# Performance work log

Measured on AMD Instinct MI355X. Metric: run time of the kernel, lower is better.

Reference implementation:

```python
import jax, jax.numpy as jnp
import numpy as np

HIDDEN = 1024
NUM_HEADS = 16
HEAD_DIM = HIDDEN // NUM_HEADS


def setup_inputs() -> dict:
    key = jax.random.key(0)
    ks = jax.random.split(key, 10)
    B, T, S = 2, 2048, 2048
    sc = 1.0 / np.sqrt(HIDDEN)
    inp = {
        "tgt": jax.random.normal(ks[0], (B, T, HIDDEN), jnp.float32),
        "src": jax.random.normal(ks[1], (B, S, HIDDEN), jnp.float32),
        # per-head projection weights stacked: [H, in_dim, head_dim]
        "Wq": jax.random.normal(ks[2], (NUM_HEADS, HIDDEN, HEAD_DIM), jnp.float32) * sc,
        "bq": jnp.zeros((NUM_HEADS, HEAD_DIM), jnp.float32),
        "Wk": jax.random.normal(ks[3], (NUM_HEADS, HIDDEN, HEAD_DIM), jnp.float32) * sc,
        "bk": jnp.zeros((NUM_HEADS, HEAD_DIM), jnp.float32),
        "Wv": jax.random.normal(ks[4], (NUM_HEADS, HIDDEN, HEAD_DIM), jnp.float32) * sc,
        "bv": jnp.zeros((NUM_HEADS, HEAD_DIM), jnp.float32),
        "Wo": jax.random.normal(ks[5], (HIDDEN, HIDDEN), jnp.float32) * sc,
        "bo": jnp.zeros((HIDDEN,), jnp.float32),
    }
    return inp


def reference(tgt, src, Wq, bq, Wk, bk, Wv, bv, Wo, bo):
    # Per-head linear projections (vectorized over heads)
    q = jnp.einsum("btd,hdk->bhtk", tgt, Wq) + bq[None, :, None, :]  # [B,H,T,Dh]
    k = jnp.einsum("bsd,hdk->bhsk", src, Wk) + bk[None, :, None, :]  # [B,H,S,Dh]
    v = jnp.einsum("bsd,hdk->bhsk", src, Wv) + bv[None, :, None, :]  # [B,H,S,Dh]
    scale = 1.0 / jnp.sqrt(jnp.asarray(HEAD_DIM, q.dtype))
    scores = jnp.einsum("bhtk,bhsk->bhts", q, k) * scale  # [B,H,T,S]
    weights = jax.nn.softmax(scores, axis=-1)
    out = jnp.einsum("bhts,bhsk->bhtk", weights, v)  # [B,H,T,Dh]
    # concat heads along last dim (head order matches torch cat)
    B, H, T, Dh = out.shape
    h = out.transpose(0, 2, 1, 3).reshape(B, T, H * Dh)
    return h @ Wo + bo
```

## Files before the change

kernel.cpp:

```cpp
#include <hip/hip_runtime.h>

typedef _Float16 f16;
typedef __attribute__((ext_vector_type(4))) _Float16 f16x4;
typedef __attribute__((ext_vector_type(8))) _Float16 f16x8;
typedef __attribute__((ext_vector_type(4))) float f32x4;

constexpr int HID = 1024, NH = 16, DH = 64, BB = 2, TT = 2048, SS = 2048;
constexpr float SCL = 0.18033688011112042f;

__device__ __forceinline__ void gl_lds16(const void* g, void* l) {
  __builtin_amdgcn_global_load_lds(
      (const __attribute__((address_space(1))) void*)g,
      (__attribute__((address_space(3))) void*)l, 16, 0, 0);
}

#define VMCNT(N) asm volatile("s_waitcnt vmcnt(" #N ")" ::: "memory")

#if __has_builtin(__builtin_amdgcn_exp2f)
#define EXP2(x) __builtin_amdgcn_exp2f(x)
#else
#define EXP2(x) exp2f(x)
#endif

__global__ __launch_bounds__(256) void k_cvt_act_all(
    const float* __restrict__ tgt, const float* __restrict__ src,
    f16* __restrict__ tgt16, f16* __restrict__ src16) {
  const int n_each = BB * TT * HID;
  int i = (blockIdx.x * 256 + threadIdx.x) * 8;
  const float* in = tgt;
  f16* out = tgt16;
  if (i >= n_each) { in = src; out = src16; i -= n_each; }
  float4 a = *(const float4*)(in + i);
  float4 b = *(const float4*)(in + i + 4);
  f16x8 o;
  o[0] = (f16)a.x; o[1] = (f16)a.y; o[2] = (f16)a.z; o[3] = (f16)a.w;
  o[4] = (f16)b.x; o[5] = (f16)b.y; o[6] = (f16)b.z; o[7] = (f16)b.w;
  *(f16x8*)(out + i) = o;
}

__global__ __launch_bounds__(256) void k_cvt_w_all(
    const float* __restrict__ Wq, const float* __restrict__ Wk,
    const float* __restrict__ Wv, const float* __restrict__ Wo,
    f16* __restrict__ wq16, f16* __restrict__ wk16, f16* __restrict__ wv16,
    f16* __restrict__ wo16) {
  __shared__ f16 t[64 * 72];
  const int x = blockIdx.x, wsel = x >> 8, idx = x & 255;
  const float* in;
  f16* out;
  int C, c0, d0, slab;
  float scale = 1.0f;
  if (wsel < 3) {
    in = (wsel == 0) ? Wq : ((wsel == 1) ? Wk : Wv);
    out = (wsel == 0) ? wq16 : ((wsel == 1) ? wk16 : wv16);
    if (wsel == 0) scale = SCL;
    C = 64; c0 = 0; d0 = (idx & 15) * 64; slab = idx >> 4;
  } else {
    in = Wo; out = wo16;
    C = 1024; c0 = (idx & 15) * 64; d0 = (idx >> 4) * 64; slab = 0;
  }
  const float* ip = in + (size_t)slab * 1024 * C;
  int tid = threadIdx.x;
  int r = tid >> 4, cq = (tid & 15) * 4;
  for (int rr = 0; rr < 64; rr += 16) {
    float4 v = *(const float4*)(ip + (size_t)(d0 + r + rr) * C + (c0 + cq));
    t[(cq + 0) * 72 + r + rr] = (f16)(v.x * scale);
    t[(cq + 1) * 72 + r + rr] = (f16)(v.y * scale);
    t[(cq + 2) * 72 + r + rr] = (f16)(v.z * scale);
    t[(cq + 3) * 72 + r + rr] = (f16)(v.w * scale);
  }
  __syncthreads();
  int c = tid >> 2, dq = (tid & 3) * 16;
  f16* op = out + (size_t)(slab * C + c0 + c) * 1024 + d0 + dq;
  *(f16x8*)op = *(const f16x8*)&t[c * 72 + dq];
  *(f16x8*)(op + 8) = *(const f16x8*)&t[c * 72 + dq + 8];
}

__global__ __launch_bounds__(256) void k_gemm_qkv(
    const f16* __restrict__ tgt16, const f16* __restrict__ src16,
    const f16* __restrict__ wq, const f16* __restrict__ wk,
    const f16* __restrict__ wv, const float* __restrict__ bq,
    const float* __restrict__ bk, const float* __restrict__ bv,
    f16* __restrict__ Qo, f16* __restrict__ Ko, f16* __restrict__ Vo) {
  __shared__ f16 lA[2][128 * 64];
  __shared__ f16 lB[2][128 * 64];
  const int tid = threadIdx.x;
  const int lane = tid & 63, hi = lane >> 4, t16 = lane & 15;
  const int w = tid >> 6;
  const int wr = (w >> 1) * 64, wc = (w & 1) * 64;
  const int i = blockIdx.x;
  const int xcd = i & 7, j = i >> 3;
  const int z = j >> 5, r = j & 31;
  const int m0 = (xcd * 4 + (r & 3)) * 128, n0 = (r >> 2) * 128;
  const f16* A = z ? src16 : tgt16;
  const f16* Bt = (z == 0) ? wq : ((z == 1) ? wk : wv);
  const float* bias = (z == 0) ? bq : ((z == 1) ? bk : bv);
  const float bscale = (z == 0) ? SCL : 1.0f;

  f32x4 acc[4][4];
#pragma unroll
  for (int a = 0; a < 4; a++)
#pragma unroll
    for (int bb = 0; bb < 4; bb++) acc[a][bb] = (f32x4){0.f, 0.f, 0.f, 0.f};

  auto STAGE = [&](int s, int kt) {
#pragma unroll
    for (int it = 0; it < 4; ++it) {
      int u = it * 256 + tid, row = u >> 3, un = u & 7;
      int gc = kt * 64 + ((un ^ (row & 7)) << 3);
      gl_lds16(A + (size_t)(m0 + row) * 1024 + gc, (char*)&lA[s][0] + u * 16);
      gl_lds16(Bt + (size_t)(n0 + row) * 1024 + gc, (char*)&lB[s][0] + u * 16);
    }
  };

  STAGE(0, 0);
  VMCNT(0);
  __builtin_amdgcn_s_barrier();
  int cur = 0;
  for (int kt = 0; kt < 16; ++kt) {
    if (kt < 15) STAGE(cur ^ 1, kt + 1);
#pragma unroll
    for (int ks = 0; ks < 2; ++ks) {
      f16x8 af[4], bf[4];
#pragma unroll
      for (int mi = 0; mi < 4; mi++) {
        int rr = wr + mi * 16 + t16;
        af[mi] = *(const f16x8*)&lA[cur][rr * 64 + (((ks * 4 + hi) ^ (rr & 7)) << 3)];
      }
#pragma unroll
      for (int ni = 0; ni < 4; ni++) {
        int rr = wc + ni * 16 + t16;
        bf[ni] = *(const f16x8*)&lB[cur][rr * 64 + (((ks * 4 + hi) ^ (rr & 7)) << 3)];
      }
      __builtin_amdgcn_s_setprio(1);
#pragma unroll
      for (int mi = 0; mi < 4; mi++)
#pragma unroll
        for (int ni = 0; ni < 4; ni++)
          acc[mi][ni] = __builtin_amdgcn_mfma_f32_16x16x32_f16(
              af[mi], bf[ni], acc[mi][ni], 0, 0, 0);
      __builtin_amdgcn_s_setprio(0);
    }
    VMCNT(0);
    __builtin_amdgcn_s_barrier();
    cur ^= 1;
  }

  if (z < 2) {
    f16* outp = z ? Ko : Qo;
#pragma unroll
    for (int mi = 0; mi < 4; mi++)
#pragma unroll
      for (int ni = 0; ni < 4; ni++)
#pragma unroll
        for (int rg = 0; rg < 4; rg++) {
          int m = m0 + wr + mi * 16 + hi * 4 + rg;
          int n = n0 + wc + ni * 16 + t16;
          outp[(size_t)m * 1024 + n] = (f16)(acc[mi][ni][rg] + bias[n] * bscale);
        }
  } else {
#pragma unroll
    for (int mi = 0; mi < 4; mi++)
#pragma unroll
      for (int ni = 0; ni < 4; ni++)
#pragma unroll
        for (int rg = 0; rg < 4; rg++) {
          int m = m0 + wr + mi * 16 + hi * 4 + rg;
          int n = n0 + wc + ni * 16 + t16;
          int b = m >> 11, s = m & 2047;
          Vo[(((size_t)(b * NH + (n >> 6)) * DH + (n & 63)) << 11) + s] =
              (f16)(acc[mi][ni][rg] + bias[n]);
        }
  }
}

__global__ __launch_bounds__(256) void k_gemm_o(const f16* __restrict__ A,
                                                const f16* __restrict__ Bt,
                                                const float* __restrict__ bias,
                                                float* __restrict__ outp) {
  __shared__ f16 lA[2][128 * 64];
  __shared__ f16 lB[2][64 * 64];
  const int tid = threadIdx.x;
  const int lane = tid & 63, hi = lane >> 4, t16 = lane & 15;
  const int w = tid >> 6;
  const int wr = (w >> 1) * 64, wc = (w & 1) * 32;
  const int i = blockIdx.x;
  const int xcd = i & 7, j = i >> 3;
  const int m0 = (xcd * 4 + (j & 3)) * 128, n0 = (j >> 2) * 64;

  f32x4 acc[4][2];
#pragma unroll
  for (int a = 0; a < 4; a++)
#pragma unroll
    for (int bb = 0; bb < 2; bb++) acc[a][bb] = (f32x4){0.f, 0.f, 0.f, 0.f};

  auto STAGE = [&](int s, int kt) {
#pragma unroll
    for (int it = 0; it < 4; ++it) {
      int u = it * 256 + tid, row = u >> 3, un = u & 7;
      int gc = kt * 64 + ((un ^ (row & 7)) << 3);
      gl_lds16(A + (size_t)(m0 + row) * 1024 + gc, (char*)&lA[s][0] + u * 16);
    }
#pragma unroll
    for (int it = 0; it < 2; ++it) {
      int u = it * 256 + tid, row = u >> 3, un = u & 7;
      int gc = kt * 64 + ((un ^ (row & 7)) << 3);
      gl_lds16(Bt + (size_t)(n0 + row) * 1024 + gc, (char*)&lB[s][0] + u * 16);
    }
  };

  STAGE(0, 0);
  VMCNT(0);
  __builtin_amdgcn_s_barrier();
  int cur = 0;
  for (int kt = 0; kt < 16; ++kt) {
    if (kt < 15) STAGE(cur ^ 1, kt + 1);
#pragma unroll
    for (int ks = 0; ks < 2; ++ks) {
      f16x8 af[4], bf[2];
#pragma unroll
      for (int mi = 0; mi < 4; mi++) {
        int rr = wr + mi * 16 + t16;
        af[mi] = *(const f16x8*)&lA[cur][rr * 64 + (((ks * 4 + hi) ^ (rr & 7)) << 3)];
      }
#pragma unroll
      for (int ni = 0; ni < 2; ni++) {
        int rr = wc + ni * 16 + t16;
        bf[ni] = *(const f16x8*)&lB[cur][rr * 64 + (((ks * 4 + hi) ^ (rr & 7)) << 3)];
      }
      __builtin_amdgcn_s_setprio(1);
#pragma unroll
      for (int mi = 0; mi < 4; mi++)
#pragma unroll
        for (int ni = 0; ni < 2; ni++)
          acc[mi][ni] = __builtin_amdgcn_mfma_f32_16x16x32_f16(
              af[mi], bf[ni], acc[mi][ni], 0, 0, 0);
      __builtin_amdgcn_s_setprio(0);
    }
    VMCNT(0);
    __builtin_amdgcn_s_barrier();
    cur ^= 1;
  }

#pragma unroll
  for (int mi = 0; mi < 4; mi++)
#pragma unroll
    for (int ni = 0; ni < 2; ni++)
#pragma unroll
      for (int rg = 0; rg < 4; rg++) {
        int m = m0 + wr + mi * 16 + hi * 4 + rg;
        int n = n0 + wc + ni * 16 + t16;
        outp[(size_t)m * 1024 + n] = acc[mi][ni][rg] + bias[n];
      }
}

__global__ __launch_bounds__(256) void k_attn(const f16* __restrict__ Q,
                                              const f16* __restrict__ K,
                                              const f16* __restrict__ Vt,
                                              f16* __restrict__ Hout) {
  __shared__ f16 lK[3][64 * 64];
  __shared__ f16 lV[3][64 * 64];
  const int tid = threadIdx.x;
  const int lane = tid & 63, hi = lane >> 4, t16 = lane & 15;
  const int w = tid >> 6;
  const int id = blockIdx.y * 16 + blockIdx.x;
  const int bh = (id & 7) * 4 + ((id >> 3) & 3);
  const int b = bh >> 4, h = bh & 15;
  const int tq = (id >> 5) * 128 + w * 32;

  f16x8 qa[2][2];
#pragma unroll
  for (int g = 0; g < 2; ++g)
#pragma unroll
    for (int ks = 0; ks < 2; ++ks)
      qa[g][ks] = *(const f16x8*)(Q + (size_t)(b * TT + tq + g * 16 + t16) * HID +
                                  h * DH + ks * 32 + hi * 8);
#pragma unroll
  for (int g = 0; g < 2; ++g)
#pragma unroll
    for (int ks = 0; ks < 2; ++ks) asm volatile("" : "+v"(qa[g][ks]));

  float lrow[2] = {0.f, 0.f};
  f32x4 o[2][4];
#pragma unroll
  for (int g = 0; g < 2; ++g)
#pragma unroll
    for (int dc = 0; dc < 4; ++dc) o[g][dc] = (f32x4){0.f, 0.f, 0.f, 0.f};

  auto STAGE = [&](int s, int sb) {
#pragma unroll
    for (int it = 0; it < 2; ++it) {
      int u = it * 256 + tid, row = u >> 3, un = u & 7;
      int kc = (un ^ (row & 7)) << 3;
      gl_lds16(K + (size_t)(b * SS + sb * 64 + row) * HID + h * DH + kc,
               (char*)&lK[s][0] + u * 16);
      gl_lds16(Vt + ((size_t)(b * NH + h) * DH + row) * SS + sb * 64 + kc,
               (char*)&lV[s][0] + u * 16);
    }
  };

  STAGE(0, 0);
  STAGE(1, 1);
  int cs = 0;
  for (int i = 0; i < 32; ++i) {
    if (i < 31) { VMCNT(4); } else { VMCNT(0); }
    __builtin_amdgcn_s_barrier();
    __builtin_amdgcn_sched_barrier(0);
    int ns = cs + 2; if (ns >= 3) ns -= 3;
    if (i + 2 < 32) STAGE(ns, i + 2);

    f16x8 kb[4][2];
#pragma unroll
    for (int sb = 0; sb < 4; ++sb) {
      int r = sb * 16 + t16;
#pragma unroll
      for (int ks = 0; ks < 2; ++ks)
        kb[sb][ks] = *(const f16x8*)&lK[cs][r * 64 + (((ks * 4 + hi) ^ (r & 7)) << 3)];
    }
    f32x4 sc[4][2];
#pragma unroll
    for (int sb = 0; sb < 4; ++sb)
#pragma unroll
      for (int g = 0; g < 2; ++g) sc[sb][g] = (f32x4){0.f, 0.f, 0.f, 0.f};
    __builtin_amdgcn_s_setprio(1);
#pragma unroll
    for (int sb = 0; sb < 4; ++sb)
#pragma unroll
      for (int g = 0; g < 2; ++g)
#pragma unroll
        for (int ks = 0; ks < 2; ++ks)
          sc[sb][g] = __builtin_amdgcn_mfma_f32_16x16x32_f16(
              kb[sb][ks], qa[g][ks], sc[sb][g], 0, 0, 0);
    __builtin_amdgcn_s_setprio(0);

    f16x4 pf[2][4];
#pragma unroll
    for (int g = 0; g < 2; ++g) {
#pragma unroll
      for (int sb = 0; sb < 4; ++sb) {
        float p0 = EXP2(sc[sb][g][0]);
        float p1 = EXP2(sc[sb][g][1]);
        float p2 = EXP2(sc[sb][g][2]);
        float p3 = EXP2(sc[sb][g][3]);
        lrow[g] += (p0 + p1) + (p2 + p3);
        f16x4 pv; pv[0] = (f16)p0; pv[1] = (f16)p1; pv[2] = (f16)p2; pv[3] = (f16)p3;
        pf[g][sb] = pv;
      }
    }

    f16x4 vf[4][4];
#pragma unroll
    for (int dc = 0; dc < 4; ++dc) {
#pragma unroll
      for (int sk = 0; sk < 4; ++sk) {
        int chunk = ((2 * sk + (hi >> 1)) ^ (t16 & 7));
        vf[dc][sk] = *(const f16x4*)&lV[cs][(dc * 16 + t16) * 64 + chunk * 8 + (hi & 1) * 4];
      }
    }

    __builtin_amdgcn_s_setprio(1);
#pragma unroll
    for (int g = 0; g < 2; ++g)
#pragma unroll
      for (int dc = 0; dc < 4; ++dc)
#pragma unroll
        for (int sk = 0; sk < 4; ++sk)
          o[g][dc] = __builtin_amdgcn_mfma_f32_16x16x16f16(vf[dc][sk], pf[g][sk],
                                                           o[g][dc], 0, 0, 0);
    __builtin_amdgcn_s_setprio(0);

    cs = (cs == 2) ? 0 : cs + 1;
  }

#pragma unroll
  for (int g = 0; g < 2; ++g) {
    float l = lrow[g];
    l += __shfl_xor(l, 16);
    l += __shfl_xor(l, 32);
    float rinv = 1.0f / l;
#pragma unroll
    for (int dc = 0; dc < 4; ++dc) {
      f16x4 ov;
#pragma unroll
      for (int rg = 0; rg < 4; ++rg) ov[rg] = (f16)(o[g][dc][rg] * rinv);
      *(f16x4*)(Hout + (size_t)(b * TT + tq + g * 16 + t16) * HID + h * DH +
                dc * 16 + hi * 4) = ov;
    }
  }
}

extern "C" void kernel_launch(void* const* d_in, const int* in_sizes, int n_in,
                              void* d_out, int out_size, void* d_ws, size_t ws_size,
                              hipStream_t stream) {
  const float* tgt = (const float*)d_in[0];
  const float* src = (const float*)d_in[1];
  const float* Wq = (const float*)d_in[2];
  const float* bq = (const float*)d_in[3];
  const float* Wk = (const float*)d_in[4];
  const float* bk = (const float*)d_in[5];
  const float* Wv = (const float*)d_in[6];
  const float* bv = (const float*)d_in[7];
  const float* Wo = (const float*)d_in[8];
  const float* bo = (const float*)d_in[9];
  float* out = (float*)d_out;

  char* ws = (char*)d_ws;
  f16* tgt16 = (f16*)(ws);
  f16* src16 = (f16*)(ws + (8u << 20));
  f16* wq16 = (f16*)(ws + (16u << 20));
  f16* wk16 = (f16*)(ws + (18u << 20));
  f16* wv16 = (f16*)(ws + (20u << 20));
  f16* wo16 = (f16*)(ws + (22u << 20));
  f16* Q16 = (f16*)(ws + (24u << 20));
  f16* K16 = (f16*)(ws + (32u << 20));
  f16* Vt16 = (f16*)(ws + (40u << 20));
  f16* h16 = (f16*)(ws + (48u << 20));

  k_cvt_act_all<<<4096, 256, 0, stream>>>(tgt, src, tgt16, src16);
  k_cvt_w_all<<<1024, 256, 0, stream>>>(Wq, Wk, Wv, Wo, wq16, wk16, wv16, wo16);

  k_gemm_qkv<<<768, 256, 0, stream>>>(tgt16, src16, wq16, wk16, wv16,
                                      bq, bk, bv, Q16, K16, Vt16);

  k_attn<<<dim3(16, 32), 256, 0, stream>>>(Q16, K16, Vt16, h16);

  k_gemm_o<<<512, 256, 0, stream>>>(h16, wo16, bo, out);
}
```

Measured before the change: 212.7 us.

## Merge convert kernels, shrink QKV GEMM N-tile, use 128-key double-buffered attention tiles

Three separate changes. The activation and weight fp16 conversion kernels become one launch, removing a kernel boundary. The QKV GEMM tile goes from 128x128 to 128x64, doubling the grid to 1536 blocks for better CU occupancy and load balance at the cost of more A-tile reloads. The attention kernel switches from a 3-stage 64-key pipeline to a 2-stage 128-key double buffer with one barrier per 128 keys. That fills LDS with larger tiles, possibly lowering occupancy, and the loads get less prefetch lead time.

```diff
diff --git a/kernel.cpp b/kernel.cpp
--- a/kernel.cpp
+++ b/kernel.cpp
@@ -22,29 +22,29 @@
 #define EXP2(x) exp2f(x)
 #endif
 
-__global__ __launch_bounds__(256) void k_cvt_act_all(
+__global__ __launch_bounds__(256) void k_cvt_all(
     const float* __restrict__ tgt, const float* __restrict__ src,
-    f16* __restrict__ tgt16, f16* __restrict__ src16) {
-  const int n_each = BB * TT * HID;
-  int i = (blockIdx.x * 256 + threadIdx.x) * 8;
-  const float* in = tgt;
-  f16* out = tgt16;
-  if (i >= n_each) { in = src; out = src16; i -= n_each; }
-  float4 a = *(const float4*)(in + i);
-  float4 b = *(const float4*)(in + i + 4);
-  f16x8 o;
-  o[0] = (f16)a.x; o[1] = (f16)a.y; o[2] = (f16)a.z; o[3] = (f16)a.w;
-  o[4] = (f16)b.x; o[5] = (f16)b.y; o[6] = (f16)b.z; o[7] = (f16)b.w;
-  *(f16x8*)(out + i) = o;
-}
-
-__global__ __launch_bounds__(256) void k_cvt_w_all(
     const float* __restrict__ Wq, const float* __restrict__ Wk,
     const float* __restrict__ Wv, const float* __restrict__ Wo,
-    f16* __restrict__ wq16, f16* __restrict__ wk16, f16* __restrict__ wv16,
-    f16* __restrict__ wo16) {
+    f16* __restrict__ tgt16, f16* __restrict__ src16, f16* __restrict__ wq16,
+    f16* __restrict__ wk16, f16* __restrict__ wv16, f16* __restrict__ wo16) {
   __shared__ f16 t[64 * 72];
-  const int x = blockIdx.x, wsel = x >> 8, idx = x & 255;
+  const int bx = blockIdx.x;
+  if (bx < 4096) {
+    const int n_each = BB * TT * HID;
+    int i = (bx * 256 + threadIdx.x) * 8;
+    const float* in = tgt;
+    f16* out = tgt16;
+    if (i >= n_each) { in = src; out = src16; i -= n_each; }
+    float4 a = *(const float4*)(in + i);
+    float4 b = *(const float4*)(in + i + 4);
+    f16x8 o;
+    o[0] = (f16)a.x; o[1] = (f16)a.y; o[2] = (f16)a.z; o[3] = (f16)a.w;
+    o[4] = (f16)b.x; o[5] = (f16)b.y; o[6] = (f16)b.z; o[7] = (f16)b.w;
+    *(f16x8*)(out + i) = o;
+    return;
+  }
+  const int x = bx - 4096, wsel = x >> 8, idx = x & 255;
   const float* in;
   f16* out;
   int C, c0, d0, slab;
@@ -82,25 +82,25 @@
     const float* __restrict__ bk, const float* __restrict__ bv,
     f16* __restrict__ Qo, f16* __restrict__ Ko, f16* __restrict__ Vo) {
   __shared__ f16 lA[2][128 * 64];
-  __shared__ f16 lB[2][128 * 64];
+  __shared__ f16 lB[2][64 * 64];
   const int tid = threadIdx.x;
   const int lane = tid & 63, hi = lane >> 4, t16 = lane & 15;
   const int w = tid >> 6;
-  const int wr = (w >> 1) * 64, wc = (w & 1) * 64;
+  const int wr = (w >> 1) * 64, wc = (w & 1) * 32;
   const int i = blockIdx.x;
   const int xcd = i & 7, j = i >> 3;
-  const int z = j >> 5, r = j & 31;
-  const int m0 = (xcd * 4 + (r & 3)) * 128, n0 = (r >> 2) * 128;
+  const int z = j >> 6, r = j & 63;
+  const int m0 = (xcd * 4 + (r & 3)) * 128, n0 = (r >> 2) * 64;
   const f16* A = z ? src16 : tgt16;
   const f16* Bt = (z == 0) ? wq : ((z == 1) ? wk : wv);
   const float* bias = (z == 0) ? bq : ((z == 1) ? bk : bv);
   const float bscale = (z == 0) ? SCL : 1.0f;
 
-  f32x4 acc[4][4];
+  f32x4 acc[4][2];
 #pragma unroll
   for (int a = 0; a < 4; a++)
 #pragma unroll
-    for (int bb = 0; bb < 4; bb++) acc[a][bb] = (f32x4){0.f, 0.f, 0.f, 0.f};
+    for (int bb = 0; bb < 2; bb++) acc[a][bb] = (f32x4){0.f, 0.f, 0.f, 0.f};
 
   auto STAGE = [&](int s, int kt) {
 #pragma unroll
@@ -108,6 +108,11 @@
       int u = it * 256 + tid, row = u >> 3, un = u & 7;
       int gc = kt * 64 + ((un ^ (row & 7)) << 3);
       gl_lds16(A + (size_t)(m0 + row) * 1024 + gc, (char*)&lA[s][0] + u * 16);
+    }
+#pragma unroll
+    for (int it = 0; it < 2; ++it) {
+      int u = it * 256 + tid, row = u >> 3, un = u & 7;
+      int gc = kt * 64 + ((un ^ (row & 7)) << 3);
       gl_lds16(Bt + (size_t)(n0 + row) * 1024 + gc, (char*)&lB[s][0] + u * 16);
     }
   };
@@ -120,14 +125,14 @@
     if (kt < 15) STAGE(cur ^ 1, kt + 1);
 #pragma unroll
     for (int ks = 0; ks < 2; ++ks) {
-      f16x8 af[4], bf[4];
+      f16x8 af[4], bf[2];
 #pragma unroll
       for (int mi = 0; mi < 4; mi++) {
         int rr = wr + mi * 16 + t16;
         af[mi] = *(const f16x8*)&lA[cur][rr * 64 + (((ks * 4 + hi) ^ (rr & 7)) << 3)];
       }
 #pragma unroll
-      for (int ni = 0; ni < 4; ni++) {
+      for (int ni = 0; ni < 2; ni++) {
         int rr = wc + ni * 16 + t16;
         bf[ni] = *(const f16x8*)&lB[cur][rr * 64 + (((ks * 4 + hi) ^ (rr & 7)) << 3)];
       }
@@ -135,7 +140,7 @@
 #pragma unroll
       for (int mi = 0; mi < 4; mi++)
 #pragma unroll
-        for (int ni = 0; ni < 4; ni++)
+        for (int ni = 0; ni < 2; ni++)
           acc[mi][ni] = __builtin_amdgcn_mfma_f32_16x16x32_f16(
               af[mi], bf[ni], acc[mi][ni], 0, 0, 0);
       __builtin_amdgcn_s_setprio(0);
@@ -150,7 +155,7 @@
 #pragma unroll
     for (int mi = 0; mi < 4; mi++)
 #pragma unroll
-      for (int ni = 0; ni < 4; ni++)
+      for (int ni = 0; ni < 2; ni++)
 #pragma unroll
         for (int rg = 0; rg < 4; rg++) {
           int m = m0 + wr + mi * 16 + hi * 4 + rg;
@@ -161,7 +166,7 @@
 #pragma unroll
     for (int mi = 0; mi < 4; mi++)
 #pragma unroll
-      for (int ni = 0; ni < 4; ni++)
+      for (int ni = 0; ni < 2; ni++)
 #pragma unroll
         for (int rg = 0; rg < 4; rg++) {
           int m = m0 + wr + mi * 16 + hi * 4 + rg;
@@ -257,8 +262,8 @@
                                               const f16* __restrict__ K,
                                               const f16* __restrict__ Vt,
                                               f16* __restrict__ Hout) {
-  __shared__ f16 lK[3][64 * 64];
-  __shared__ f16 lV[3][64 * 64];
+  __shared__ f16 lK[2][128 * 64];
+  __shared__ f16 lV[2][64 * 128];
   const int tid = threadIdx.x;
   const int lane = tid & 63, hi = lane >> 4, t16 = lane & 15;
   const int w = tid >> 6;
@@ -286,89 +291,95 @@
 #pragma unroll
     for (int dc = 0; dc < 4; ++dc) o[g][dc] = (f32x4){0.f, 0.f, 0.f, 0.f};
 
-  auto STAGE = [&](int s, int sb) {
-#pragma unroll
-    for (int it = 0; it < 2; ++it) {
+  auto STAGE = [&](int s, int tb) {
+#pragma unroll
+    for (int it = 0; it < 4; ++it) {
       int u = it * 256 + tid, row = u >> 3, un = u & 7;
       int kc = (un ^ (row & 7)) << 3;
-      gl_lds16(K + (size_t)(b * SS + sb * 64 + row) * HID + h * DH + kc,
+      gl_lds16(K + (size_t)(b * SS + tb * 128 + row) * HID + h * DH + kc,
                (char*)&lK[s][0] + u * 16);
-      gl_lds16(Vt + ((size_t)(b * NH + h) * DH + row) * SS + sb * 64 + kc,
+    }
+#pragma unroll
+    for (int it = 0; it < 4; ++it) {
+      int u = it * 256 + tid, d = u >> 4, un = u & 15;
+      int scol = ((un & 8) | ((un & 7) ^ (d & 7))) << 3;
+      gl_lds16(Vt + ((size_t)(b * NH + h) * DH + d) * SS + tb * 128 + scol,
                (char*)&lV[s][0] + u * 16);
     }
   };
 
   STAGE(0, 0);
-  STAGE(1, 1);
-  int cs = 0;
-  for (int i = 0; i < 32; ++i) {
-    if (i < 31) { VMCNT(4); } else { VMCNT(0); }
+  VMCNT(0);
+  __builtin_amdgcn_s_barrier();
+  int cur = 0;
+  for (int t = 0; t < 16; ++t) {
+    if (t < 15) STAGE(cur ^ 1, t + 1);
+#pragma unroll
+    for (int hs = 0; hs < 2; ++hs) {
+      f16x8 kb[4][2];
+#pragma unroll
+      for (int sb = 0; sb < 4; ++sb) {
+        int r = hs * 64 + sb * 16 + t16;
+#pragma unroll
+        for (int ks = 0; ks < 2; ++ks)
+          kb[sb][ks] = *(const f16x8*)&lK[cur][r * 64 + (((ks * 4 + hi) ^ (r & 7)) << 3)];
+      }
+      f32x4 sc[4][2];
+#pragma unroll
+      for (int sb = 0; sb < 4; ++sb)
+#pragma unroll
+        for (int g = 0; g < 2; ++g) sc[sb][g] = (f32x4){0.f, 0.f, 0.f, 0.f};
+      __builtin_amdgcn_s_setprio(1);
+#pragma unroll
+      for (int sb = 0; sb < 4; ++sb)
+#pragma unroll
+        for (int g = 0; g < 2; ++g)
+#pragma unroll
+          for (int ks = 0; ks < 2; ++ks)
+            sc[sb][g] = __builtin_amdgcn_mfma_f32_16x16x32_f16(
+                kb[sb][ks], qa[g][ks], sc[sb][g], 0, 0, 0);
+      __builtin_amdgcn_s_setprio(0);
+
+      f16x4 pf[2][4];
+#pragma unroll
+      for (int g = 0; g < 2; ++g) {
+#pragma unroll
+        for (int sb = 0; sb < 4; ++sb) {
+          float p0 = EXP2(sc[sb][g][0]);
+          float p1 = EXP2(sc[sb][g][1]);
+          float p2 = EXP2(sc[sb][g][2]);
+          float p3 = EXP2(sc[sb][g][3]);
+          lrow[g] += (p0 + p1) + (p2 + p3);
+          f16x4 pv; pv[0] = (f16)p0; pv[1] = (f16)p1; pv[2] = (f16)p2; pv[3] = (f16)p3;
+          pf[g][sb] = pv;
+        }
+      }
+
+      f16x4 vf[4][4];
+#pragma unroll
+      for (int dc = 0; dc < 4; ++dc) {
+#pragma unroll
+        for (int sk = 0; sk < 4; ++sk) {
+          int chunk = ((2 * sk + (hi >> 1)) ^ (t16 & 7));
+          vf[dc][sk] = *(const f16x4*)&lV[cur][(dc * 16 + t16) * 128 + hs * 64 +
+                                               chunk * 8 + (hi & 1) * 4];
+        }
+      }
+
+      __builtin_amdgcn_s_setprio(1);
+#pragma unroll
+      for (int g = 0; g < 2; ++g)
+#pragma unroll
+        for (int dc = 0; dc < 4; ++dc)
+#pragma unroll
+          for (int sk = 0; sk < 4; ++sk)
+            o[g][dc] = __builtin_amdgcn_mfma_f32_16x16x16f16(vf[dc][sk], pf[g][sk],
+                                                             o[g][dc], 0, 0, 0);
+      __builtin_amdgcn_s_setprio(0);
+    }
+    VMCNT(0);
     __builtin_amdgcn_s_barrier();
-    __builtin_amdgcn_sched_barrier(0);
-    int ns = cs + 2; if (ns >= 3) ns -= 3;
-    if (i + 2 < 32) STAGE(ns, i + 2);
-
-    f16x8 kb[4][2];
-#pragma unroll
-    for (int sb = 0; sb < 4; ++sb) {
-      int r = sb * 16 + t16;
-#pragma unroll
-      for (int ks = 0; ks < 2; ++ks)
-        kb[sb][ks] = *(const f16x8*)&lK[cs][r * 64 + (((ks * 4 + hi) ^ (r & 7)) << 3)];
-    }
-    f32x4 sc[4][2];
-#pragma unroll
-    for (int sb = 0; sb < 4; ++sb)
-#pragma unroll
-      for (int g = 0; g < 2; ++g) sc[sb][g] = (f32x4){0.f, 0.f, 0.f, 0.f};
-    __builtin_amdgcn_s_setprio(1);
-#pragma unroll
-    for (int sb = 0; sb < 4; ++sb)
-#pragma unroll
-      for (int g = 0; g < 2; ++g)
-#pragma unroll
-        for (int ks = 0; ks < 2; ++ks)
-          sc[sb][g] = __builtin_amdgcn_mfma_f32_16x16x32_f16(
-              kb[sb][ks], qa[g][ks], sc[sb][g], 0, 0, 0);
-    __builtin_amdgcn_s_setprio(0);
-
-    f16x4 pf[2][4];
-#pragma unroll
-    for (int g = 0; g < 2; ++g) {
-#pragma unroll
-      for (int sb = 0; sb < 4; ++sb) {
-        float p0 = EXP2(sc[sb][g][0]);
-        float p1 = EXP2(sc[sb][g][1]);
-        float p2 = EXP2(sc[sb][g][2]);
-        float p3 = EXP2(sc[sb][g][3]);
-        lrow[g] += (p0 + p1) + (p2 + p3);
-        f16x4 pv; pv[0] = (f16)p0; pv[1] = (f16)p1; pv[2] = (f16)p2; pv[3] = (f16)p3;
-        pf[g][sb] = pv;
-      }
-    }
-
-    f16x4 vf[4][4];
-#pragma unroll
-    for (int dc = 0; dc < 4; ++dc) {
-#pragma unroll
-      for (int sk = 0; sk < 4; ++sk) {
-        int chunk = ((2 * sk + (hi >> 1)) ^ (t16 & 7));
-        vf[dc][sk] = *(const f16x4*)&lV[cs][(dc * 16 + t16) * 64 + chunk * 8 + (hi & 1) * 4];
-      }
-    }
-
-    __builtin_amdgcn_s_setprio(1);
-#pragma unroll
-    for (int g = 0; g < 2; ++g)
-#pragma unroll
-      for (int dc = 0; dc < 4; ++dc)
-#pragma unroll
-        for (int sk = 0; sk < 4; ++sk)
-          o[g][dc] = __builtin_amdgcn_mfma_f32_16x16x16f16(vf[dc][sk], pf[g][sk],
-                                                           o[g][dc], 0, 0, 0);
-    __builtin_amdgcn_s_setprio(0);
-
-    cs = (cs == 2) ? 0 : cs + 1;
+    cur ^= 1;
   }
 
 #pragma unroll
@@ -415,11 +426,11 @@
   f16* Vt16 = (f16*)(ws + (40u << 20));
   f16* h16 = (f16*)(ws + (48u << 20));
 
-  k_cvt_act_all<<<4096, 256, 0, stream>>>(tgt, src, tgt16, src16);
-  k_cvt_w_all<<<1024, 256, 0, stream>>>(Wq, Wk, Wv, Wo, wq16, wk16, wv16, wo16);
-
-  k_gemm_qkv<<<768, 256, 0, stream>>>(tgt16, src16, wq16, wk16, wv16,
-                                      bq, bk, bv, Q16, K16, Vt16);
+  k_cvt_all<<<5120, 256, 0, stream>>>(tgt, src, Wq, Wk, Wv, Wo,
+                                      tgt16, src16, wq16, wk16, wv16, wo16);
+
+  k_gemm_qkv<<<1536, 256, 0, stream>>>(tgt16, src16, wq16, wk16, wv16,
+                                       bq, bk, bv, Q16, K16, Vt16);
 
   k_attn<<<dim3(16, 32), 256, 0, stream>>>(Q16, K16, Vt16, h16);
 
```

After: 207.9 us. 2.3% less time.
